# Kernel tuning notes

Measured on AMD Instinct MI355X. Metric: run time of the kernel, lower is better.

## Reference

```python
import jax, jax.numpy as jnp
import numpy as np

B, CZ, E, V, H, W = 256, 512, 512, 4096, 16, 16  # batch, z_channels, embed_dim, vocab, latent HxW


def setup_inputs() -> dict:
    key = jax.random.key(0)
    k0, k1, k2, k3 = jax.random.split(key, 4)
    x = jax.random.normal(k0, (B, CZ, H, W), jnp.float32)          # encoder feature map
    pre_w = jax.random.normal(k1, (E, CZ), jnp.float32) * 0.02     # 1x1 pre_quant_conv weight
    pre_b = jnp.zeros((E,), jnp.float32)
    emb = jax.random.uniform(k2, (V, E), jnp.float32, -1.0 / V, 1.0 / V)  # codebook, uniform init as in module
    post_w = jax.random.normal(k3, (CZ, E), jnp.float32) * 0.02    # 1x1 post_quant_conv weight
    post_b = jnp.zeros((CZ,), jnp.float32)
    return dict(x=x, pre_w=pre_w, pre_b=pre_b, emb=emb, post_w=post_w, post_b=post_b)


def reference(x, pre_w, pre_b, emb, post_w, post_b):
    # pre_quant_conv: 1x1 Conv2d(CZ -> E)
    z = jnp.einsum('bchw,ec->behw', x, pre_w) + pre_b[None, :, None, None]
    b, e, h, w = z.shape
    # flatten spatial: (b h w, e)
    zf = z.transpose(0, 2, 3, 1).reshape(-1, e)
    # expanded squared-distance to codebook: ||z||^2 + ||c||^2 - 2 z.c
    dist = (jnp.sum(zf * zf, axis=1, keepdims=True)
            + jnp.sum(emb * emb, axis=1)
            - 2.0 * zf @ emb.T)                                    # [bhw, V]
    tokens = jnp.argmin(dist, axis=-1)                             # [bhw] int
    z_q = emb[tokens].reshape(b, h, w, e).transpose(0, 3, 1, 2)    # gather -> [b,e,h,w]
    # straight-through estimator
    dec_in = z + jax.lax.stop_gradient(z_q - z)
    # post_quant_conv: 1x1 Conv2d(E -> CZ)
    rec = jnp.einsum('behw,ce->bchw', dec_in, post_w) + post_b[None, :, None, None]
    return z, z_q, rec
```

## Files before the change

kernel.cpp:

```cpp
#include <hip/hip_runtime.h>
#include <hip/hip_bf16.h>

typedef unsigned short u16;
typedef unsigned char  u8;
typedef unsigned int   u32;
typedef unsigned long long u64;
typedef long long ll;

using short8 = __attribute__((ext_vector_type(8))) short;
using f32x4  = __attribute__((ext_vector_type(4))) float;
using u16x8  = __attribute__((ext_vector_type(8))) unsigned short;
using ll2    = __attribute__((ext_vector_type(2))) long long;

#define AS_GLOBAL __attribute__((address_space(1)))
#define AS_LDS    __attribute__((address_space(3)))

__device__ __forceinline__ u16 f2b(float x){
  u32 u = __float_as_uint(x);
  u32 r = (u + 0x7FFFu + ((u >> 16) & 1u)) >> 16;
  return (u16)r;
}
__device__ __forceinline__ float b2f(u16 h){ return __uint_as_float(((u32)h) << 16); }

__device__ __forceinline__ u32 f2e4m3(float x){
  float ax = fabsf(x);
  u32 s = (__float_as_uint(x) & 0x80000000u) >> 24;
  ax = fminf(ax, 448.0f);
  if (ax < 0.015625f){
    u32 m = (u32)__float2int_rn(ax * 512.0f);
    return s | m;
  }
  u32 u = __float_as_uint(ax);
  u32 man = u & 0x7FFFFFu;
  u32 rnd = man + 0x7FFFFu + ((man >> 20) & 1u);
  u32 e = (u >> 23) + (rnd >> 23);
  u32 m = (rnd >> 23) ? 0u : ((rnd >> 20) & 7u);
  if (e > 135u) return s | 0x7Eu;
  return s | ((e - 120u) << 3) | m;
}

__device__ __forceinline__ void gload16(u16* l, const u16* g){
  __builtin_amdgcn_global_load_lds((const AS_GLOBAL u32*)g, (AS_LDS u32*)l, 16, 0, 0);
}

__device__ __forceinline__ u64 umin64(u64 a, u64 b){ return a < b ? a : b; }

__device__ __forceinline__ u64 shfl_xor_u64(u64 v, int m){
  u32 lo = __shfl_xor((u32)v, m, 64);
  u32 hi = __shfl_xor((u32)(v >> 32), m, 64);
  return ((u64)hi << 32) | lo;
}

__global__ void k_cvt(const float* __restrict__ w, u16* __restrict__ d, int n){
  int i = blockIdx.x * 256 + threadIdx.x;
  if (i < n) d[i] = f2b(w[i]);
}

__global__ void k_cvt8(const float* __restrict__ src, u8* __restrict__ dst){
  int id = blockIdx.x * 256 + threadIdx.x;
  int row = id >> 7, db = id & 127;
  int b0 = db * 4;
  int kb = b0 >> 6, r6 = b0 & 63;
  int g = r6 >> 4, ks = (r6 >> 3) & 1, j0 = r6 & 7;
  int k = kb * 64 + ks * 32 + g * 8 + j0;
  const float* p = src + (size_t)row * 512 + k;
  u32 w = f2e4m3(p[0] * 1048576.0f)
        | (f2e4m3(p[1] * 1048576.0f) << 8)
        | (f2e4m3(p[2] * 1048576.0f) << 16)
        | (f2e4m3(p[3] * 1048576.0f) << 24);
  *(u32*)(dst + (size_t)row * 512 + b0) = w;
}

__global__ void k_cnorm(const float* __restrict__ emb, float* __restrict__ cn26){
  int v = blockIdx.x, lane = threadIdx.x;
  const float* r = emb + (size_t)v * 512;
  float s = 0.f;
  #pragma unroll
  for (int i = 0; i < 8; ++i){ float x = r[lane + i * 64]; s += x * x; }
  #pragma unroll
  for (int off = 32; off; off >>= 1) s += __shfl_down(s, off, 64);
  if (lane == 0) cn26[v] = s * 67108864.0f;
}

__global__ void k_tcvt(const float* __restrict__ src, u16* __restrict__ d){
  __shared__ float t[64][65];
  const int bid = blockIdx.x;
  const int b  = bid >> 5;
  const int rb = (bid >> 2) & 7;
  const int cb = bid & 3;
  const float* s = src + ((size_t)b * 512 + (size_t)rb * 64) * 256 + cb * 64;
  const int tid = threadIdx.x;
  #pragma unroll
  for (int j = 0; j < 4; ++j){
    int fl = j * 256 + tid;
    int r = fl >> 4, c4 = (fl & 15) * 4;
    float4 v = *(const float4*)(s + (size_t)r * 256 + c4);
    t[r][c4 + 0] = v.x; t[r][c4 + 1] = v.y; t[r][c4 + 2] = v.z; t[r][c4 + 3] = v.w;
  }
  __syncthreads();
  u16* o = d + ((size_t)b * 256 + (size_t)cb * 64) * 512 + rb * 64;
  #pragma unroll
  for (int j = 0; j < 2; ++j){
    int fl = j * 256 + tid;
    int c = fl >> 3, r8 = (fl & 7) * 8;
    u16x8 hv;
    #pragma unroll
    for (int i = 0; i < 8; ++i) hv[i] = f2b(t[r8 + i][c]);
    *(u16x8*)(o + (size_t)c * 512 + r8) = hv;
  }
}

__global__ void k_zq(const u64* __restrict__ keys, const float* __restrict__ emb, float* __restrict__ zq){
  int sidx = blockIdx.x * 64 + threadIdx.x;
  int b = sidx >> 8, s = sidx & 255;
  int v = (int)(u32)keys[sidx];
  const float4* er = (const float4*)(emb + (size_t)v * 512);
  float* o = zq + (size_t)b * 512 * 256 + s;
  #pragma unroll 4
  for (int e4 = 0; e4 < 128; ++e4){
    float4 vv = er[e4];
    o[(size_t)(e4 * 4 + 0) * 256] = vv.x;
    o[(size_t)(e4 * 4 + 1) * 256] = vv.y;
    o[(size_t)(e4 * 4 + 2) * 256] = vv.z;
    o[(size_t)(e4 * 4 + 3) * 256] = vv.w;
  }
}

template<int MODE>
__global__ __launch_bounds__(256, 4) void k_gemm(
    const u16* __restrict__ Ah,
    const u16* __restrict__ Bh,
    const u64* __restrict__ gkeys,
    const float* __restrict__ bias,
    float* __restrict__ Cout,
    u8* __restrict__ Z8,
    int M, int mtbits)
{
  constexpr int K = 512;
  __shared__ __align__(16) u16 sA[128 * 64];
  __shared__ __align__(16) u16 sB[128 * 64];

  const int tid  = threadIdx.x;
  const int lane = tid & 63;
  const int wid  = tid >> 6;
  const int wm = wid >> 1, wn = wid & 1;

  const int nwg = gridDim.x;
  const int chunk = nwg >> 3;
  const int pb = blockIdx.x;
  const int bid = (pb & 7) * chunk + (pb >> 3);

  const int mt = bid & ((1 << mtbits) - 1);
  const int nt = (bid >> mtbits) & 1;
  const int b  = bid >> (mtbits + 1);
  const int m0 = mt * 128;
  const int n0 = nt * 128;
  const int bbase = b * 256;

  const u16* ga[4];
  const u16* gb[4];
  int ldso[4];
  #pragma unroll
  for (int i = 0; i < 4; ++i){
    int e = i * 256 + tid;
    int r = e >> 3;
    int sl = (e & 7) ^ (r & 7);
    ldso[i] = e * 8;
    ga[i] = Ah + (size_t)(m0 + r) * K + sl * 8;
    size_t brow;
    if (MODE == 2) brow = (size_t)(u32)gkeys[bbase + n0 + r];
    else           brow = (size_t)(bbase + n0 + r);
    gb[i] = Bh + brow * K + sl * 8;
  }

  const f32x4 zero4 = {0.f, 0.f, 0.f, 0.f};
  f32x4 acc[4][4];
  #pragma unroll
  for (int i = 0; i < 4; ++i)
    #pragma unroll
    for (int j = 0; j < 4; ++j) acc[i][j] = zero4;

  int aoff[2][4], boff[2][4];
  #pragma unroll
  for (int ks = 0; ks < 2; ++ks)
    #pragma unroll
    for (int f = 0; f < 4; ++f){
      int rA = wm * 64 + f * 16 + (lane & 15);
      aoff[ks][f] = rA * 64 + (((ks * 4 + (lane >> 4)) ^ (rA & 7)) * 8);
      int rB = wn * 64 + f * 16 + (lane & 15);
      boff[ks][f] = rB * 64 + (((ks * 4 + (lane >> 4)) ^ (rB & 7)) * 8);
    }

  for (int kt = 0; kt < 8; ++kt){
    const int k0 = kt * 64;
    #pragma unroll
    for (int i = 0; i < 4; ++i){
      gload16(&sA[ldso[i]], ga[i] + k0);
      gload16(&sB[ldso[i]], gb[i] + k0);
    }
    __syncthreads();
    #pragma unroll
    for (int ks = 0; ks < 2; ++ks){
      short8 ah[4], bh[4];
      #pragma unroll
      for (int f = 0; f < 4; ++f){
        ah[f] = *(const short8*)&sA[aoff[ks][f]];
        bh[f] = *(const short8*)&sB[boff[ks][f]];
      }
      #pragma unroll
      for (int fm = 0; fm < 4; ++fm)
        #pragma unroll
        for (int fn = 0; fn < 4; ++fn)
          acc[fm][fn] = __builtin_amdgcn_mfma_f32_16x16x32_bf16(ah[fm], bh[fn], acc[fm][fn], 0, 0, 0);
    }
    __syncthreads();
  }

  const int row0 = m0 + wm * 64;
  const int col  = n0 + wn * 64 + (lane & 15);
  float* Cb = Cout + (size_t)b * M * 256;
  #pragma unroll
  for (int fm = 0; fm < 4; ++fm){
    #pragma unroll
    for (int j = 0; j < 4; ++j){
      int row = row0 + fm * 16 + (lane >> 4) * 4 + j;
      float bi = bias[row];
      #pragma unroll
      for (int fn = 0; fn < 4; ++fn)
        Cb[(size_t)row * 256 + col + fn * 16] = acc[fm][fn][j] + bi;
    }
  }

  if (MODE == 0){
    #pragma unroll
    for (int fm = 0; fm < 4; ++fm){
      int rb4 = row0 + fm * 16 + (lane >> 4) * 4;
      int pb0 = (rb4 >> 6) * 64 + (((rb4 >> 3) & 3) * 16) + (((rb4 >> 5) & 1) * 8) + (rb4 & 7);
      float bi0 = bias[rb4], bi1 = bias[rb4+1], bi2 = bias[rb4+2], bi3 = bias[rb4+3];
      #pragma unroll
      for (int fn = 0; fn < 4; ++fn){
        u32 w = f2e4m3((acc[fm][fn][0] + bi0) * 64.0f)
              | (f2e4m3((acc[fm][fn][1] + bi1) * 64.0f) << 8)
              | (f2e4m3((acc[fm][fn][2] + bi2) * 64.0f) << 16)
              | (f2e4m3((acc[fm][fn][3] + bi3) * 64.0f) << 24);
        *(u32*)(Z8 + (size_t)(bbase + col + fn * 16) * 512 + pb0) = w;
      }
    }
  }
}

__global__ __launch_bounds__(512, 1) void k_gemm2(
    const u8* __restrict__ A8,
    const u8* __restrict__ B8,
    const float* __restrict__ cn26,
    u64* __restrict__ okeys)
{
  __shared__ __align__(16) u8 lds[163840];

  const int tid  = threadIdx.x;
  const int lane = tid & 63;
  const int wid  = tid >> 6;
  const int wm   = wid >> 2;
  const int wn   = wid & 3;
  const int b    = blockIdx.x;
  const int bbase = b * 256;
  const int g4   = lane >> 4;

#define SB    __builtin_amdgcn_sched_barrier(0)
#define BAR   __builtin_amdgcn_s_barrier()
#define LGKM0 asm volatile("s_waitcnt lgkmcnt(0)" ::: "memory")
#define VM2   asm volatile("s_waitcnt vmcnt(2)" ::: "memory")
#define VM0   asm volatile("s_waitcnt vmcnt(0)" ::: "memory")

  #pragma unroll
  for (int i = 0; i < 16; ++i){
    int e = i * 512 + tid;
    int t = e >> 5, s = e & 31;
    gload16((u16*)&lds[e * 16],
            (const u16*)(B8 + (size_t)(bbase + t) * 512 + ((s ^ (t & 31)) * 16)));
  }

  const u8* gsrcA0 = A8 + (size_t)(tid >> 2) * 512 + (tid & 3) * 16;
  const u8* gsrcA1 = gsrcA0 + 65536;

#define STG_A(tp) { const size_t _o = (size_t)((tp) >> 3) * 131072 + ((tp) & 7) * 64; \
    const int _d = 131072 + ((tp) & 1) * 16384; \
    gload16((u16*)&lds[_d + tid * 16], (const u16*)(gsrcA0 + _o)); \
    gload16((u16*)&lds[_d + 8192 + tid * 16], (const u16*)(gsrcA1 + _o)); }

  int aBase[8];
  #pragma unroll
  for (int fm = 0; fm < 8; ++fm)
    aBase[fm] = 131072 + (wm * 128 + fm * 16 + (lane & 15)) * 64 + g4 * 16;
  int tB[4], mB[4];
  #pragma unroll
  for (int fn = 0; fn < 4; ++fn){
    tB[fn] = wn * 64 + fn * 16 + (lane & 15);
    mB[fn] = tB[fn] & 31;
  }

  const f32x4 zero4 = {0.f, 0.f, 0.f, 0.f};
  f32x4 acc[8][4];
  #pragma unroll
  for (int i = 0; i < 8; ++i)
    #pragma unroll
    for (int j = 0; j < 4; ++j) acc[i][j] = zero4;

  u64 best[4];
  #pragma unroll
  for (int i = 0; i < 4; ++i) best[i] = ~0ull;

  STG_A(0)

  for (int mt = 0; mt < 16; ++mt){
    #pragma unroll
    for (int kt = 0; kt < 8; ++kt){
      const int tau = mt * 8 + kt;
      if (tau < 127) STG_A(tau + 1)
      if (tau == 127){ VM0; } else { VM2; }
      SB; BAR; SB;

      const int bufo = (tau & 1) * 16384;
      ll2 af[8], bv[4];
      #pragma unroll
      for (int fm = 0; fm < 8; ++fm)
        af[fm] = *(const ll2*)&lds[aBase[fm] + bufo];
      #pragma unroll
      for (int fn = 0; fn < 4; ++fn)
        bv[fn] = *(const ll2*)&lds[tB[fn] * 512 + (((kt * 4 + g4) ^ mB[fn]) * 16)];
      LGKM0; SB; BAR; SB;

      __builtin_amdgcn_s_setprio(1);
      #pragma unroll
      for (int fm = 0; fm < 8; ++fm)
        #pragma unroll
        for (int fn = 0; fn < 4; ++fn){
          acc[fm][fn] = __builtin_amdgcn_mfma_f32_16x16x32_fp8_fp8(af[fm][0], bv[fn][0], acc[fm][fn], 0, 0, 0);
          acc[fm][fn] = __builtin_amdgcn_mfma_f32_16x16x32_fp8_fp8(af[fm][1], bv[fn][1], acc[fm][fn], 0, 0, 0);
        }
      __builtin_amdgcn_s_setprio(0);
      SB;
    }

    {
      const float4* cp = (const float4*)(cn26 + mt * 256 + wm * 128 + g4 * 4);
      float4 cnr[8];
      #pragma unroll
      for (int fm = 0; fm < 8; ++fm) cnr[fm] = cp[fm * 4];
      VM0;
      #pragma unroll
      for (int fn = 0; fn < 4; ++fn){
        #pragma unroll
        for (int fm = 0; fm < 8; ++fm){
          #pragma unroll
          for (int jj = 0; jj < 4; ++jj){
            int v = mt * 256 + wm * 128 + fm * 16 + g4 * 4 + jj;
            float sc = ((const float*)&cnr[fm])[jj] - 2.0f * acc[fm][fn][jj];
            u32 o = __float_as_uint(sc);
            o = (o & 0x80000000u) ? ~o : (o | 0x80000000u);
            best[fn] = umin64(best[fn], ((u64)o << 32) | (u32)v);
          }
        }
      }
      #pragma unroll
      for (int i = 0; i < 8; ++i)
        #pragma unroll
        for (int jj = 0; jj < 4; ++jj) acc[i][jj] = zero4;
    }
  }

  #pragma unroll
  for (int fn = 0; fn < 4; ++fn){
    best[fn] = umin64(best[fn], shfl_xor_u64(best[fn], 16));
    best[fn] = umin64(best[fn], shfl_xor_u64(best[fn], 32));
  }
  __syncthreads();
  u64* kbuf = (u64*)&lds[131072];
  if (lane < 16){
    #pragma unroll
    for (int fn = 0; fn < 4; ++fn)
      kbuf[wm * 256 + wn * 64 + fn * 16 + lane] = best[fn];
  }
  __syncthreads();
  if (tid < 256)
    okeys[bbase + tid] = umin64(kbuf[tid], kbuf[256 + tid]);

#undef STG_A
#undef SB
#undef BAR
#undef LGKM0
#undef VM2
#undef VM0
}

extern "C" void kernel_launch(void* const* d_in, const int* in_sizes, int n_in,
                              void* d_out, int out_size, void* d_ws, size_t ws_size,
                              hipStream_t stream){
  const float* x      = (const float*)d_in[0];
  const float* pre_w  = (const float*)d_in[1];
  const float* pre_b  = (const float*)d_in[2];
  const float* emb    = (const float*)d_in[3];
  const float* post_w = (const float*)d_in[4];
  const float* post_b = (const float*)d_in[5];

  float* z_out   = (float*)d_out;
  float* zq_out  = z_out + 33554432;
  float* rec_out = z_out + 67108864;

  char* w = (char*)d_ws;
  u16* prew_b  = (u16*)(w);
  u16* postw_b = (u16*)(w + 524288);
  u16* emb_b   = (u16*)(w + 1048576);
  u8*  emb8    = (u8*)(w + 5242880);
  float* cn26  = (float*)(w + 7340032);
  u64* keys    = (u64*)(w + 7356416);
  u16* xb      = (u16*)(w + 7880704);
  u8*  z8      = (u8*)(w + 74989568);

  k_cvt  <<<1024, 256, 0, stream>>>(pre_w, prew_b, 262144);
  k_cvt  <<<1024, 256, 0, stream>>>(post_w, postw_b, 262144);
  k_cvt  <<<8192, 256, 0, stream>>>(emb, emb_b, 2097152);
  k_cvt8 <<<2048, 256, 0, stream>>>(emb, emb8);
  k_cnorm<<<4096, 64, 0, stream>>>(emb, cn26);

  k_tcvt<<<8192, 256, 0, stream>>>(x, xb);

  k_gemm<0><<<256 * 2 * 4, 256, 0, stream>>>(prew_b, xb,
      nullptr, pre_b, z_out, z8, 512, 2);

  k_gemm2<<<256, 512, 0, stream>>>(emb8, z8, cn26, keys);

  k_zq<<<1024, 64, 0, stream>>>(keys, emb, zq_out);

  k_gemm<2><<<256 * 2 * 4, 256, 0, stream>>>(postw_b, emb_b,
      keys, post_b, rec_out, nullptr, 512, 2);
}
```

Before: 574.2 us.

## Load codebook A fragments directly from global into registers, drop LDS staging

The distance GEMM kernel stops staging codebook (A) tiles in double-buffered LDS with barriers. Each wave now loads its A fragments straight from global memory into registers, using a two-register-set ping-pong to prefetch the next k-step while running MFMAs on the current one. The per-codebook norm vector is preloaded into LDS once instead of being read from global each m-tile. This removes per-k-step barriers and LDS traffic for A, but makes every wave fetch A redundantly from global/L2 (the four wn waves share rows) and relies on the compiler to hide global latency without explicit waitcnt scheduling.

```diff
diff --git a/kernel.cpp b/kernel.cpp
--- a/kernel.cpp
+++ b/kernel.cpp
@@ -255,7 +255,7 @@
     const float* __restrict__ cn26,
     u64* __restrict__ okeys)
 {
-  __shared__ __align__(16) u8 lds[163840];
+  __shared__ __align__(16) u8 lds[151552];
 
   const int tid  = threadIdx.x;
   const int lane = tid & 63;
@@ -266,12 +266,6 @@
   const int bbase = b * 256;
   const int g4   = lane >> 4;
 
-#define SB    __builtin_amdgcn_sched_barrier(0)
-#define BAR   __builtin_amdgcn_s_barrier()
-#define LGKM0 asm volatile("s_waitcnt lgkmcnt(0)" ::: "memory")
-#define VM2   asm volatile("s_waitcnt vmcnt(2)" ::: "memory")
-#define VM0   asm volatile("s_waitcnt vmcnt(0)" ::: "memory")
-
   #pragma unroll
   for (int i = 0; i < 16; ++i){
     int e = i * 512 + tid;
@@ -279,25 +273,29 @@
     gload16((u16*)&lds[e * 16],
             (const u16*)(B8 + (size_t)(bbase + t) * 512 + ((s ^ (t & 31)) * 16)));
   }
-
-  const u8* gsrcA0 = A8 + (size_t)(tid >> 2) * 512 + (tid & 3) * 16;
-  const u8* gsrcA1 = gsrcA0 + 65536;
-
-#define STG_A(tp) { const size_t _o = (size_t)((tp) >> 3) * 131072 + ((tp) & 7) * 64; \
-    const int _d = 131072 + ((tp) & 1) * 16384; \
-    gload16((u16*)&lds[_d + tid * 16], (const u16*)(gsrcA0 + _o)); \
-    gload16((u16*)&lds[_d + 8192 + tid * 16], (const u16*)(gsrcA1 + _o)); }
-
-  int aBase[8];
-  #pragma unroll
-  for (int fm = 0; fm < 8; ++fm)
-    aBase[fm] = 131072 + (wm * 128 + fm * 16 + (lane & 15)) * 64 + g4 * 16;
-  int tB[4], mB[4];
-  #pragma unroll
-  for (int fn = 0; fn < 4; ++fn){
-    tB[fn] = wn * 64 + fn * 16 + (lane & 15);
-    mB[fn] = tB[fn] & 31;
-  }
+  {
+    const float4* c4 = (const float4*)cn26;
+    float4 v0 = c4[tid], v1 = c4[tid + 512];
+    *(float4*)&lds[131072 + tid * 16] = v0;
+    *(float4*)&lds[131072 + (tid + 512) * 16] = v1;
+  }
+  asm volatile("s_waitcnt vmcnt(0)" ::: "memory");
+  __syncthreads();
+
+  const u32 abase = (u32)((wm * 128 + (lane & 15)) * 512 + g4 * 16);
+
+#define LOAD_A(dst, tau_) { const u32 o_ = ((((tau_) & 127) >> 3) * 131072u) + (((tau_) & 7) * 64u); \
+    _Pragma("unroll") for (int fm = 0; fm < 8; ++fm) \
+      dst[fm] = *(const ll2*)(A8 + abase + fm * 8192u + o_); }
+#define READ_B(kt_) { _Pragma("unroll") for (int fn = 0; fn < 4; ++fn){ \
+    int t_ = wn * 64 + fn * 16 + (lane & 15); \
+    bv[fn] = *(const ll2*)&lds[t_ * 512 + ((((kt_) * 4 + g4) ^ (t_ & 31)) * 16)]; } }
+#define MM(af) { __builtin_amdgcn_s_setprio(1); \
+  _Pragma("unroll") for (int fm = 0; fm < 8; ++fm) \
+    _Pragma("unroll") for (int fn = 0; fn < 4; ++fn){ \
+      acc[fm][fn] = __builtin_amdgcn_mfma_f32_16x16x32_fp8_fp8(af[fm][0], bv[fn][0], acc[fm][fn], 0, 0, 0); \
+      acc[fm][fn] = __builtin_amdgcn_mfma_f32_16x16x32_fp8_fp8(af[fm][1], bv[fn][1], acc[fm][fn], 0, 0, 0); } \
+  __builtin_amdgcn_s_setprio(0); }
 
   const f32x4 zero4 = {0.f, 0.f, 0.f, 0.f};
   f32x4 acc[8][4];
@@ -310,52 +308,32 @@
   #pragma unroll
   for (int i = 0; i < 4; ++i) best[i] = ~0ull;
 
-  STG_A(0)
+  ll2 afA[8], afB[8], bv[4];
+  LOAD_A(afA, 0)
 
   for (int mt = 0; mt < 16; ++mt){
     #pragma unroll
-    for (int kt = 0; kt < 8; ++kt){
-      const int tau = mt * 8 + kt;
-      if (tau < 127) STG_A(tau + 1)
-      if (tau == 127){ VM0; } else { VM2; }
-      SB; BAR; SB;
-
-      const int bufo = (tau & 1) * 16384;
-      ll2 af[8], bv[4];
-      #pragma unroll
-      for (int fm = 0; fm < 8; ++fm)
-        af[fm] = *(const ll2*)&lds[aBase[fm] + bufo];
-      #pragma unroll
-      for (int fn = 0; fn < 4; ++fn)
-        bv[fn] = *(const ll2*)&lds[tB[fn] * 512 + (((kt * 4 + g4) ^ mB[fn]) * 16)];
-      LGKM0; SB; BAR; SB;
-
-      __builtin_amdgcn_s_setprio(1);
-      #pragma unroll
-      for (int fm = 0; fm < 8; ++fm)
-        #pragma unroll
-        for (int fn = 0; fn < 4; ++fn){
-          acc[fm][fn] = __builtin_amdgcn_mfma_f32_16x16x32_fp8_fp8(af[fm][0], bv[fn][0], acc[fm][fn], 0, 0, 0);
-          acc[fm][fn] = __builtin_amdgcn_mfma_f32_16x16x32_fp8_fp8(af[fm][1], bv[fn][1], acc[fm][fn], 0, 0, 0);
-        }
-      __builtin_amdgcn_s_setprio(0);
-      SB;
+    for (int kp = 0; kp < 4; ++kp){
+      const int tau = mt * 8 + kp * 2;
+      LOAD_A(afB, tau + 1)
+      READ_B(kp * 2)
+      MM(afA)
+      LOAD_A(afA, tau + 2)
+      READ_B(kp * 2 + 1)
+      MM(afB)
     }
 
     {
-      const float4* cp = (const float4*)(cn26 + mt * 256 + wm * 128 + g4 * 4);
-      float4 cnr[8];
-      #pragma unroll
-      for (int fm = 0; fm < 8; ++fm) cnr[fm] = cp[fm * 4];
-      VM0;
+      const int cnb = 131072 + (mt * 256 + wm * 128 + g4 * 4) * 4;
       #pragma unroll
       for (int fn = 0; fn < 4; ++fn){
         #pragma unroll
         for (int fm = 0; fm < 8; ++fm){
+          float4 cnr = *(const float4*)&lds[cnb + fm * 64];
           #pragma unroll
           for (int jj = 0; jj < 4; ++jj){
             int v = mt * 256 + wm * 128 + fm * 16 + g4 * 4 + jj;
-            float sc = ((const float*)&cnr[fm])[jj] - 2.0f * acc[fm][fn][jj];
+            float sc = ((const float*)&cnr)[jj] - 2.0f * acc[fm][fn][jj];
             u32 o = __float_as_uint(sc);
             o = (o & 0x80000000u) ? ~o : (o | 0x80000000u);
             best[fn] = umin64(best[fn], ((u64)o << 32) | (u32)v);
@@ -375,7 +353,7 @@
     best[fn] = umin64(best[fn], shfl_xor_u64(best[fn], 32));
   }
   __syncthreads();
-  u64* kbuf = (u64*)&lds[131072];
+  u64* kbuf = (u64*)&lds[147456];
   if (lane < 16){
     #pragma unroll
     for (int fn = 0; fn < 4; ++fn)
@@ -385,12 +363,9 @@
   if (tid < 256)
     okeys[bbase + tid] = umin64(kbuf[tid], kbuf[256 + tid]);
 
-#undef STG_A
-#undef SB
-#undef BAR
-#undef LGKM0
-#undef VM2
-#undef VM0
+#undef LOAD_A
+#undef READ_B
+#undef MM
 }
 
 extern "C" void kernel_launch(void* const* d_in, const int* in_sizes, int n_in,
```

Result: slower. 811.3 us (+41.3%).

## Restructure FP8 codebook GEMM pipeline with register double-buffering and one barrier per step

Applied to the files above, without the earlier changes.

The main argmin GEMM loop is reorganised. Global-to-LDS staging of codebook tiles now runs two steps ahead. A-fragments are double-buffered in registers (afA/afB), so LDS reads for the next step are issued before the MFMAs of the current step. This cuts the per-k-step synchronisation from two barriers to one. The A tile in LDS also gets a rotation swizzle to reduce bank conflicts, and B addresses are precomputed with XOR. The cost is more VGPR pressure from the second fragment set, a full vmcnt(0) wait every step, and a few out-of-range wrap-around prefetches at the tail.

```diff
diff --git a/kernel.cpp b/kernel.cpp
--- a/kernel.cpp
+++ b/kernel.cpp
@@ -5,7 +5,6 @@
 typedef unsigned char  u8;
 typedef unsigned int   u32;
 typedef unsigned long long u64;
-typedef long long ll;
 
 using short8 = __attribute__((ext_vector_type(8))) short;
 using f32x4  = __attribute__((ext_vector_type(4))) float;
@@ -269,8 +268,8 @@
 #define SB    __builtin_amdgcn_sched_barrier(0)
 #define BAR   __builtin_amdgcn_s_barrier()
 #define LGKM0 asm volatile("s_waitcnt lgkmcnt(0)" ::: "memory")
+#define VM0   asm volatile("s_waitcnt vmcnt(0)" ::: "memory")
 #define VM2   asm volatile("s_waitcnt vmcnt(2)" ::: "memory")
-#define VM0   asm volatile("s_waitcnt vmcnt(0)" ::: "memory")
 
   #pragma unroll
   for (int i = 0; i < 16; ++i){
@@ -280,24 +279,38 @@
             (const u16*)(B8 + (size_t)(bbase + t) * 512 + ((s ^ (t & 31)) * 16)));
   }
 
-  const u8* gsrcA0 = A8 + (size_t)(tid >> 2) * 512 + (tid & 3) * 16;
-  const u8* gsrcA1 = gsrcA0 + 65536;
-
-#define STG_A(tp) { const size_t _o = (size_t)((tp) >> 3) * 131072 + ((tp) & 7) * 64; \
-    const int _d = 131072 + ((tp) & 1) * 16384; \
-    gload16((u16*)&lds[_d + tid * 16], (const u16*)(gsrcA0 + _o)); \
-    gload16((u16*)&lds[_d + 8192 + tid * 16], (const u16*)(gsrcA1 + _o)); }
-
-  int aBase[8];
-  #pragma unroll
-  for (int fm = 0; fm < 8; ++fm)
-    aBase[fm] = 131072 + (wm * 128 + fm * 16 + (lane & 15)) * 64 + g4 * 16;
-  int tB[4], mB[4];
+  const u8* gA0; const u8* gA1;
+  {
+    int r0 = tid >> 2, s0 = tid & 3;
+    gA0 = A8 + (size_t)r0 * 512 + (((s0 - (r0 >> 1)) & 3) * 16);
+    int e1 = tid + 512, r1 = e1 >> 2, s1 = e1 & 3;
+    gA1 = A8 + (size_t)r1 * 512 + (((s1 - (r1 >> 1)) & 3) * 16);
+  }
+
+#define STG_A(tau_) { const u32 o_ = (u32)((((tau_) >> 3) & 15) * 131072) + (u32)(((tau_) & 7) * 64); \
+    const int d_ = 131072 + (((tau_) & 1) * 16384); \
+    gload16((u16*)&lds[d_ + tid * 16], (const u16*)(gA0 + o_)); \
+    gload16((u16*)&lds[d_ + 8192 + tid * 16], (const u16*)(gA1 + o_)); }
+
+  const int aOff = 131072 + wm * 8192 + (lane & 15) * 64
+                 + (((g4 + ((lane & 15) >> 1)) & 3) * 16);
+  int bB0[4];
   #pragma unroll
   for (int fn = 0; fn < 4; ++fn){
-    tB[fn] = wn * 64 + fn * 16 + (lane & 15);
-    mB[fn] = tB[fn] & 31;
-  }
+    int t_ = wn * 64 + fn * 16 + (lane & 15);
+    bB0[fn] = t_ * 512 + ((g4 ^ (t_ & 31)) * 16);
+  }
+
+#define READ_AF(dst, bsel) { _Pragma("unroll") for (int fm = 0; fm < 8; ++fm) \
+    dst[fm] = *(const ll2*)&lds[aOff + (bsel) * 16384 + fm * 1024]; }
+#define READ_BV(ktc) { _Pragma("unroll") for (int fn = 0; fn < 4; ++fn) \
+    bv[fn] = *(const ll2*)&lds[bB0[fn] ^ ((ktc) << 6)]; }
+#define MM(af) { __builtin_amdgcn_s_setprio(1); \
+  _Pragma("unroll") for (int fm = 0; fm < 8; ++fm) \
+    _Pragma("unroll") for (int fn = 0; fn < 4; ++fn){ \
+      acc[fm][fn] = __builtin_amdgcn_mfma_f32_16x16x32_fp8_fp8(af[fm][0], bv[fn][0], acc[fm][fn], 0, 0, 0); \
+      acc[fm][fn] = __builtin_amdgcn_mfma_f32_16x16x32_fp8_fp8(af[fm][1], bv[fn][1], acc[fm][fn], 0, 0, 0); } \
+  __builtin_amdgcn_s_setprio(0); }
 
   const f32x4 zero4 = {0.f, 0.f, 0.f, 0.f};
   f32x4 acc[8][4];
@@ -310,36 +323,25 @@
   #pragma unroll
   for (int i = 0; i < 4; ++i) best[i] = ~0ull;
 
+  ll2 afA[8], afB[8], bv[4];
+
   STG_A(0)
-
+  STG_A(1)
+  VM2; BAR; SB;
+  READ_AF(afA, 0)
+
+  #pragma unroll 1
   for (int mt = 0; mt < 16; ++mt){
     #pragma unroll
     for (int kt = 0; kt < 8; ++kt){
       const int tau = mt * 8 + kt;
-      if (tau < 127) STG_A(tau + 1)
-      if (tau == 127){ VM0; } else { VM2; }
-      SB; BAR; SB;
-
-      const int bufo = (tau & 1) * 16384;
-      ll2 af[8], bv[4];
-      #pragma unroll
-      for (int fm = 0; fm < 8; ++fm)
-        af[fm] = *(const ll2*)&lds[aBase[fm] + bufo];
-      #pragma unroll
-      for (int fn = 0; fn < 4; ++fn)
-        bv[fn] = *(const ll2*)&lds[tB[fn] * 512 + (((kt * 4 + g4) ^ mB[fn]) * 16)];
-      LGKM0; SB; BAR; SB;
-
-      __builtin_amdgcn_s_setprio(1);
-      #pragma unroll
-      for (int fm = 0; fm < 8; ++fm)
-        #pragma unroll
-        for (int fn = 0; fn < 4; ++fn){
-          acc[fm][fn] = __builtin_amdgcn_mfma_f32_16x16x32_fp8_fp8(af[fm][0], bv[fn][0], acc[fm][fn], 0, 0, 0);
-          acc[fm][fn] = __builtin_amdgcn_mfma_f32_16x16x32_fp8_fp8(af[fm][1], bv[fn][1], acc[fm][fn], 0, 0, 0);
-        }
-      __builtin_amdgcn_s_setprio(0);
+      LGKM0; VM0; SB; BAR; SB;
+      READ_BV(kt)
+      if (kt & 1){ READ_AF(afA, ((kt + 1) & 1)) }
+      else       { READ_AF(afB, ((kt + 1) & 1)) }
+      STG_A(tau + 2)
       SB;
+      if (kt & 1){ MM(afB) } else { MM(afA) }
     }
 
     {
@@ -347,7 +349,6 @@
       float4 cnr[8];
       #pragma unroll
       for (int fm = 0; fm < 8; ++fm) cnr[fm] = cp[fm * 4];
-      VM0;
       #pragma unroll
       for (int fn = 0; fn < 4; ++fn){
         #pragma unroll
@@ -386,11 +387,14 @@
     okeys[bbase + tid] = umin64(kbuf[tid], kbuf[256 + tid]);
 
 #undef STG_A
+#undef READ_AF
+#undef READ_BV
+#undef MM
 #undef SB
 #undef BAR
 #undef LGKM0
+#undef VM0
 #undef VM2
-#undef VM0
 }
 
 extern "C" void kernel_launch(void* const* d_in, const int* in_sizes, int n_in,
```

Result: slower. 690.0 us (+20.2%).
